# Kernel optimization log

Hardware: AMD Instinct MI355X
Metric: run time of the kernel (lower is better)

The kernel has to match this reference:

```python
import jax, jax.numpy as jnp
import numpy as np

L = 8        # len_prog
E = 8        # experts per layer (uniform dsl_num)
D = 256      # embed_dim
B = 16384    # batch_size
H1, H2 = 64, 32  # MyMLP hidden dims


def setup_inputs() -> dict:
    key = jax.random.key(0)
    ks = jax.random.split(key, 8)
    s1 = 1.0 / np.sqrt(D)
    s2 = 1.0 / np.sqrt(H1)
    s3 = 1.0 / np.sqrt(H2)
    return {
        "src_embeddings": jax.random.normal(ks[0], (B, D), jnp.float32),
        "W1": jax.random.normal(ks[1], (L, E, H1, D), jnp.float32) * s1,
        "b1": jax.random.normal(ks[2], (L, E, H1), jnp.float32) * s1,
        "W2": jax.random.normal(ks[3], (L, E, H2, H1), jnp.float32) * s2,
        "b2": jax.random.normal(ks[4], (L, E, H2), jnp.float32) * s2,
        "W3": jax.random.normal(ks[5], (L, E, D, H2), jnp.float32) * s3,
        "b3": jax.random.normal(ks[6], (L, E, D), jnp.float32) * s3,
        "masks": jax.random.normal(ks[7], (L, B, E), jnp.float32) * 0.1,
    }


def reference(src_embeddings, W1, b1, W2, b2, W3, b3, masks):
    # Per layer: run E small expert MLPs on the same x, then combine with
    # softmax(mask) over the expert axis (torch path: masks=None -> softmax).
    def layer(x, params):
        w1, bb1, w2, bb2, w3, bb3, m = params
        h = jax.nn.relu(jnp.einsum('bd,ehd->beh', x, w1) + bb1)      # [B,E,H1]
        h = jax.nn.relu(jnp.einsum('beh,ekh->bek', h, w2) + bb2)     # [B,E,H2]
        out = jnp.einsum('bek,edk->bed', h, w3) + bb3                # [B,E,D]
        w = jax.nn.softmax(m, axis=-1)                               # [B,E]
        x_new = jnp.einsum('be,bed->bd', w, out)                     # [B,D]
        return x_new, None

    x, _ = jax.lax.scan(layer, src_embeddings, (W1, b1, W2, b2, W3, b3, masks))
    return x
```

## Files before the change

### kernel.cpp

```cpp
#include <hip/hip_runtime.h>
#include <hip/hip_bf16.h>

#define LNUM 8
#define ENUM 8
#define DDIM 256
#define BSZ  16384
#define H1N  64
#define H2N  32

#define BT   64
#define NTHR 512

#define PX   264
#define PH1  72
#define PH2  40
#define PSW  9

#define WS1_OFF 0
#define WS2_OFF 1048576
#define WS3_OFF 1179648

typedef float f32x4 __attribute__((ext_vector_type(4)));
typedef unsigned short u16x8 __attribute__((ext_vector_type(8)));
typedef unsigned short u16x4 __attribute__((ext_vector_type(4)));
typedef __bf16 bf16x8 __attribute__((ext_vector_type(8)));

#define Z4 ((f32x4){0.f, 0.f, 0.f, 0.f})

static __device__ __forceinline__ unsigned short f2bf(float f) {
    unsigned u = __builtin_bit_cast(unsigned, f);
    u += 0x7fffu + ((u >> 16) & 1u);
    return (unsigned short)(u >> 16);
}

static __device__ __forceinline__ f32x4 mfma16(u16x8 a, u16x8 b, f32x4 c) {
    return __builtin_amdgcn_mfma_f32_16x16x32_bf16(
        __builtin_bit_cast(bf16x8, a), __builtin_bit_cast(bf16x8, b), c, 0, 0, 0);
}

__global__ __launch_bounds__(256) void cvt_w_frag(
    const float* __restrict__ w1, const float* __restrict__ w2,
    const float* __restrict__ w3, unsigned short* __restrict__ ws)
{
    int gid = blockIdx.x * 256 + threadIdx.x;
    const float* src;
    unsigned short* dst;
    if (gid < 131072) {
        int s = gid >> 11, rem = gid & 2047;
        int n = rem >> 5, kc = rem & 31;
        int nt = n >> 4, r = n & 15, kt = kc >> 2, q = kc & 3;
        src = w1 + (size_t)gid * 8;
        dst = ws + WS1_OFF + (size_t)s * 16384 + nt * 4096 + kt * 512 + (q * 16 + r) * 8;
    } else if (gid < 147456) {
        int g = gid - 131072;
        int s = g >> 8, rem = g & 255;
        int n = rem >> 3, kc = rem & 7;
        int n2 = n >> 4, r = n & 15, kt = kc >> 2, q = kc & 3;
        src = w2 + (size_t)g * 8;
        dst = ws + WS2_OFF + (size_t)s * 2048 + n2 * 1024 + kt * 512 + (q * 16 + r) * 8;
    } else {
        int g = gid - 147456;
        int s = g >> 10, rem = g & 1023;
        int n = rem >> 2, q = rem & 3;
        int nt = n >> 4, r = n & 15;
        src = w3 + (size_t)g * 8;
        dst = ws + WS3_OFF + (size_t)s * 8192 + nt * 512 + (q * 16 + r) * 8;
    }
    float4 a = *(const float4*)src;
    float4 b = *(const float4*)(src + 4);
    u16x8 p;
    p[0] = f2bf(a.x); p[1] = f2bf(a.y); p[2] = f2bf(a.z); p[3] = f2bf(a.w);
    p[4] = f2bf(b.x); p[5] = f2bf(b.y); p[6] = f2bf(b.z); p[7] = f2bf(b.w);
    *(u16x8*)dst = p;
}

__global__ __launch_bounds__(NTHR, 2) void moe_fused(
    const float* __restrict__ src, const unsigned short* __restrict__ Wf,
    const float* __restrict__ b1, const float* __restrict__ b2,
    const float* __restrict__ b3, const float* __restrict__ masks,
    float* __restrict__ out)
{
    __shared__ __align__(16) unsigned short Xlds[BT * PX];
    __shared__ __align__(16) unsigned short H1T[2][BT * PH1];
    __shared__ __align__(16) unsigned short H2T[2][BT * PH2];
    __shared__ float SWlds[BT * PSW];

    const int tid  = threadIdx.x;
    const int lane = tid & 63;
    const int w    = tid >> 6;
    const int wm   = w >> 2;
    const int wn   = w & 3;
    const int n15  = lane & 15;
    const int q    = lane >> 4;
    const int b0   = blockIdx.x * BT;

    const unsigned short* w1base = Wf + WS1_OFF + wn * 4096 + lane * 8;
    const unsigned short* w2base = Wf + WS2_OFF + wm * 1024 + lane * 8;
    const unsigned short* w3base = Wf + WS3_OFF + wn * 2048 + lane * 8;

    u16x8 xf[2][8];
    f32x4 ACC[2][4];

    auto stage_softmax = [&](int l) {
        if (tid < 64) {
            const float* mp = masks + ((size_t)l * BSZ + b0 + tid) * ENUM;
            float4 m0 = *(const float4*)mp;
            float4 m1 = *(const float4*)(mp + 4);
            float mv[8] = {m0.x, m0.y, m0.z, m0.w, m1.x, m1.y, m1.z, m1.w};
            float mx = mv[0];
            #pragma unroll
            for (int e = 1; e < 8; ++e) mx = fmaxf(mx, mv[e]);
            float s = 0.f;
            #pragma unroll
            for (int e = 0; e < 8; ++e) { mv[e] = expf(mv[e] - mx); s += mv[e]; }
            float inv = 1.f / s;
            #pragma unroll
            for (int e = 0; e < 8; ++e) SWlds[tid * PSW + e] = mv[e] * inv;
        }
    };

    auto acc_init = [&](int l) {
        const float* b3l = b3 + (size_t)l * ENUM * DDIM;
        #pragma unroll
        for (int mt = 0; mt < 2; ++mt)
            #pragma unroll
            for (int nt = 0; nt < 4; ++nt) ACC[mt][nt] = Z4;
        #pragma unroll 2
        for (int e2 = 0; e2 < ENUM; ++e2) {
            float swv[2][4];
            #pragma unroll
            for (int mt = 0; mt < 2; ++mt)
                #pragma unroll
                for (int rg = 0; rg < 4; ++rg)
                    swv[mt][rg] = SWlds[(wm*32 + mt*16 + q*4 + rg) * PSW + e2];
            #pragma unroll
            for (int nt = 0; nt < 4; ++nt) {
                float bv = b3l[e2 * DDIM + wn*64 + nt*16 + n15];
                #pragma unroll
                for (int mt = 0; mt < 2; ++mt)
                    #pragma unroll
                    for (int rg = 0; rg < 4; ++rg)
                        ACC[mt][nt][rg] += swv[mt][rg] * bv;
            }
        }
    };

    auto xf_read = [&]() {
        #pragma unroll
        for (int mt = 0; mt < 2; ++mt)
            #pragma unroll
            for (int kt = 0; kt < 8; ++kt)
                xf[mt][kt] = *(const u16x8*)
                    &Xlds[(wm*32 + mt*16 + n15) * PX + q*8 + kt*32];
    };
    auto x_write = [&]() {
        #pragma unroll
        for (int mt = 0; mt < 2; ++mt)
            #pragma unroll
            for (int nt = 0; nt < 4; ++nt)
                #pragma unroll
                for (int rg = 0; rg < 4; ++rg)
                    Xlds[(wm*32 + mt*16 + q*4 + rg) * PX + wn*64 + nt*16 + n15] =
                        f2bf(ACC[mt][nt][rg]);
    };

    #pragma unroll
    for (int i = 0; i < 4; ++i) {
        int o = (i * NTHR + tid) * 8;
        int r = o >> 8, c = o & 255;
        const float* p = src + (size_t)(b0 + r) * DDIM + c;
        float4 f0 = *(const float4*)(p);
        float4 f1 = *(const float4*)(p + 4);
        u16x8 pk;
        pk[0] = f2bf(f0.x); pk[1] = f2bf(f0.y); pk[2] = f2bf(f0.z); pk[3] = f2bf(f0.w);
        pk[4] = f2bf(f1.x); pk[5] = f2bf(f1.y); pk[6] = f2bf(f1.z); pk[7] = f2bf(f1.w);
        *(u16x8*)&Xlds[r * PX + c] = pk;
    }
    stage_softmax(0);
    __syncthreads();
    xf_read();
    acc_init(0);

    #pragma unroll 1
    for (int ss = 0; ss < LNUM * ENUM / 2; ++ss) {
        const int s0 = 2 * ss, s1 = s0 + 1;
        const int l  = s0 >> 3, e0 = s0 & 7, e1 = s1 & 7;

        u16x8 wfA[8], wfB[8], w2A[2], w2B[2];
        {
            const unsigned short* pA = w1base + (size_t)s0 * 16384;
            const unsigned short* pB = w1base + (size_t)s1 * 16384;
            #pragma unroll
            for (int kt = 0; kt < 8; ++kt) {
                wfA[kt] = *(const u16x8*)(pA + kt * 512);
                wfB[kt] = *(const u16x8*)(pB + kt * 512);
            }
            const unsigned short* q2A = w2base + (size_t)s0 * 2048;
            const unsigned short* q2B = w2base + (size_t)s1 * 2048;
            w2A[0] = *(const u16x8*)(q2A);  w2A[1] = *(const u16x8*)(q2A + 512);
            w2B[0] = *(const u16x8*)(q2B);  w2B[1] = *(const u16x8*)(q2B + 512);
        }
        const float4 bb1A = *(const float4*)(b1 + s0 * 64 + wn * 16 + q * 4);
        const float4 bb1B = *(const float4*)(b1 + s1 * 64 + wn * 16 + q * 4);
        const float4 bb2A = *(const float4*)(b2 + s0 * 32 + wm * 16 + q * 4);
        const float4 bb2B = *(const float4*)(b2 + s1 * 32 + wm * 16 + q * 4);

        f32x4 a1A[2] = {Z4, Z4}, a1B[2] = {Z4, Z4};
        #pragma unroll
        for (int kt = 0; kt < 8; ++kt) {
            a1A[0] = mfma16(wfA[kt], xf[0][kt], a1A[0]);
            a1A[1] = mfma16(wfA[kt], xf[1][kt], a1A[1]);
            a1B[0] = mfma16(wfB[kt], xf[0][kt], a1B[0]);
            a1B[1] = mfma16(wfB[kt], xf[1][kt], a1B[1]);
        }

        u16x8 w3A[4], w3B[4];
        {
            const unsigned short* p3A = w3base + (size_t)s0 * 8192;
            const unsigned short* p3B = w3base + (size_t)s1 * 8192;
            #pragma unroll
            for (int nt = 0; nt < 4; ++nt) {
                w3A[nt] = *(const u16x8*)(p3A + nt * 512);
                w3B[nt] = *(const u16x8*)(p3B + nt * 512);
            }
        }

        #pragma unroll
        for (int mt = 0; mt < 2; ++mt) {
            u16x4 pkA, pkB;
            #pragma unroll
            for (int rg = 0; rg < 4; ++rg) {
                pkA[rg] = f2bf(fmaxf(a1A[mt][rg] + bb1A[rg], 0.f));
                pkB[rg] = f2bf(fmaxf(a1B[mt][rg] + bb1B[rg], 0.f));
            }
            int row = wm*32 + mt*16 + n15;
            *(u16x4*)&H1T[0][row * PH1 + wn*16 + q*4] = pkA;
            *(u16x4*)&H1T[1][row * PH1 + wn*16 + q*4] = pkB;
        }
        __syncthreads();

        f32x4 a2A = Z4, a2B = Z4;
        {
            u16x8 hA0 = *(const u16x8*)&H1T[0][(wn*16 + n15) * PH1 + q*8];
            u16x8 hA1 = *(const u16x8*)&H1T[0][(wn*16 + n15) * PH1 + q*8 + 32];
            u16x8 hB0 = *(const u16x8*)&H1T[1][(wn*16 + n15) * PH1 + q*8];
            u16x8 hB1 = *(const u16x8*)&H1T[1][(wn*16 + n15) * PH1 + q*8 + 32];
            a2A = mfma16(w2A[0], hA0, a2A);
            a2B = mfma16(w2B[0], hB0, a2B);
            a2A = mfma16(w2A[1], hA1, a2A);
            a2B = mfma16(w2B[1], hB1, a2B);
        }
        {
            int row = wn*16 + n15;
            float swA = SWlds[row * PSW + e0];
            float swB = SWlds[row * PSW + e1];
            u16x4 pkA, pkB;
            #pragma unroll
            for (int rg = 0; rg < 4; ++rg) {
                pkA[rg] = f2bf(fmaxf(a2A[rg] + bb2A[rg], 0.f) * swA);
                pkB[rg] = f2bf(fmaxf(a2B[rg] + bb2B[rg], 0.f) * swB);
            }
            *(u16x4*)&H2T[0][row * PH2 + wm*16 + q*4] = pkA;
            *(u16x4*)&H2T[1][row * PH2 + wm*16 + q*4] = pkB;
        }
        __syncthreads();

        {
            u16x8 hA0 = *(const u16x8*)&H2T[0][(wm*32 + n15) * PH2 + q*8];
            u16x8 hA1 = *(const u16x8*)&H2T[0][(wm*32 + 16 + n15) * PH2 + q*8];
            u16x8 hB0 = *(const u16x8*)&H2T[1][(wm*32 + n15) * PH2 + q*8];
            u16x8 hB1 = *(const u16x8*)&H2T[1][(wm*32 + 16 + n15) * PH2 + q*8];
            #pragma unroll
            for (int nt = 0; nt < 4; ++nt) {
                ACC[0][nt] = mfma16(hA0, w3A[nt], ACC[0][nt]);
                ACC[1][nt] = mfma16(hA1, w3A[nt], ACC[1][nt]);
            }
            #pragma unroll
            for (int nt = 0; nt < 4; ++nt) {
                ACC[0][nt] = mfma16(hB0, w3B[nt], ACC[0][nt]);
                ACC[1][nt] = mfma16(hB1, w3B[nt], ACC[1][nt]);
            }
        }

        if (e1 == 7 && l < LNUM - 1) {
            x_write();
            __syncthreads();
            xf_read();
            stage_softmax(l + 1);
            __syncthreads();
            acc_init(l + 1);
        }
    }

    #pragma unroll
    for (int mt = 0; mt < 2; ++mt)
        #pragma unroll
        for (int nt = 0; nt < 4; ++nt)
            #pragma unroll
            for (int rg = 0; rg < 4; ++rg)
                out[(size_t)(b0 + wm*32 + mt*16 + q*4 + rg) * DDIM
                    + wn*64 + nt*16 + n15] = ACC[mt][nt][rg];
}

extern "C" void kernel_launch(void* const* d_in, const int* in_sizes, int n_in,
                              void* d_out, int out_size, void* d_ws, size_t ws_size,
                              hipStream_t stream) {
    const float* src   = (const float*)d_in[0];
    const float* W1    = (const float*)d_in[1];
    const float* b1    = (const float*)d_in[2];
    const float* W2    = (const float*)d_in[3];
    const float* b2    = (const float*)d_in[4];
    const float* W3    = (const float*)d_in[5];
    const float* b3    = (const float*)d_in[6];
    const float* masks = (const float*)d_in[7];
    float* out = (float*)d_out;
    unsigned short* ws = (unsigned short*)d_ws;

    hipLaunchKernelGGL(cvt_w_frag, dim3(832), dim3(256), 0, stream, W1, W2, W3, ws);
    hipLaunchKernelGGL(moe_fused, dim3(BSZ / BT), dim3(NTHR), 0, stream,
                       src, ws, b1, b2, b3, masks, out);
}
```

Baseline: 190.6 us.

## Halve batch tile to 32 rows and remap stage-2 waves per expert

Batch tile shrinks from 64 to 32 rows per block, so each wave now covers one 16-row m-tile instead of two. Stage 2 is rebuilt so each wave-row group handles a single expert of the pair rather than both. Launch bounds rise to 4 blocks per CU, aiming for more resident waves, lower register pressure and twice as many blocks to fill the GPU. In exchange, each block streams the full expert weights for half as many rows, which doubles global/L2 weight traffic per output row and halves MFMA reuse of every weight fragment.

```diff
diff --git a/kernel.cpp b/kernel.cpp
--- a/kernel.cpp
+++ b/kernel.cpp
@@ -8,7 +8,7 @@
 #define H1N  64
 #define H2N  32
 
-#define BT   64
+#define BT   32
 #define NTHR 512
 
 #define PX   264
@@ -74,7 +74,7 @@
     *(u16x8*)dst = p;
 }
 
-__global__ __launch_bounds__(NTHR, 2) void moe_fused(
+__global__ __launch_bounds__(NTHR, 4) void moe_fused(
     const float* __restrict__ src, const unsigned short* __restrict__ Wf,
     const float* __restrict__ b1, const float* __restrict__ b2,
     const float* __restrict__ b3, const float* __restrict__ masks,
@@ -90,19 +90,21 @@
     const int w    = tid >> 6;
     const int wm   = w >> 2;
     const int wn   = w & 3;
+    const int r2   = wn & 1;
+    const int f2   = wn >> 1;
     const int n15  = lane & 15;
     const int q    = lane >> 4;
     const int b0   = blockIdx.x * BT;
 
     const unsigned short* w1base = Wf + WS1_OFF + wn * 4096 + lane * 8;
-    const unsigned short* w2base = Wf + WS2_OFF + wm * 1024 + lane * 8;
+    const unsigned short* w2base = Wf + WS2_OFF + f2 * 1024 + lane * 8;
     const unsigned short* w3base = Wf + WS3_OFF + wn * 2048 + lane * 8;
 
-    u16x8 xf[2][8];
-    f32x4 ACC[2][4];
+    u16x8 xf[8];
+    f32x4 ACC[4];
 
     auto stage_softmax = [&](int l) {
-        if (tid < 64) {
+        if (tid < BT) {
             const float* mp = masks + ((size_t)l * BSZ + b0 + tid) * ENUM;
             float4 m0 = *(const float4*)mp;
             float4 m1 = *(const float4*)(mp + 4);
@@ -122,50 +124,39 @@
     auto acc_init = [&](int l) {
         const float* b3l = b3 + (size_t)l * ENUM * DDIM;
         #pragma unroll
-        for (int mt = 0; mt < 2; ++mt)
-            #pragma unroll
-            for (int nt = 0; nt < 4; ++nt) ACC[mt][nt] = Z4;
+        for (int nt = 0; nt < 4; ++nt) ACC[nt] = Z4;
         #pragma unroll 2
         for (int e2 = 0; e2 < ENUM; ++e2) {
-            float swv[2][4];
-            #pragma unroll
-            for (int mt = 0; mt < 2; ++mt)
-                #pragma unroll
-                for (int rg = 0; rg < 4; ++rg)
-                    swv[mt][rg] = SWlds[(wm*32 + mt*16 + q*4 + rg) * PSW + e2];
+            float swv[4];
+            #pragma unroll
+            for (int rg = 0; rg < 4; ++rg)
+                swv[rg] = SWlds[(wm*16 + q*4 + rg) * PSW + e2];
             #pragma unroll
             for (int nt = 0; nt < 4; ++nt) {
                 float bv = b3l[e2 * DDIM + wn*64 + nt*16 + n15];
                 #pragma unroll
-                for (int mt = 0; mt < 2; ++mt)
-                    #pragma unroll
-                    for (int rg = 0; rg < 4; ++rg)
-                        ACC[mt][nt][rg] += swv[mt][rg] * bv;
+                for (int rg = 0; rg < 4; ++rg)
+                    ACC[nt][rg] += swv[rg] * bv;
             }
         }
     };
 
     auto xf_read = [&]() {
         #pragma unroll
-        for (int mt = 0; mt < 2; ++mt)
-            #pragma unroll
-            for (int kt = 0; kt < 8; ++kt)
-                xf[mt][kt] = *(const u16x8*)
-                    &Xlds[(wm*32 + mt*16 + n15) * PX + q*8 + kt*32];
+        for (int kt = 0; kt < 8; ++kt)
+            xf[kt] = *(const u16x8*)&Xlds[(wm*16 + n15) * PX + q*8 + kt*32];
     };
     auto x_write = [&]() {
         #pragma unroll
-        for (int mt = 0; mt < 2; ++mt)
-            #pragma unroll
-            for (int nt = 0; nt < 4; ++nt)
-                #pragma unroll
-                for (int rg = 0; rg < 4; ++rg)
-                    Xlds[(wm*32 + mt*16 + q*4 + rg) * PX + wn*64 + nt*16 + n15] =
-                        f2bf(ACC[mt][nt][rg]);
+        for (int nt = 0; nt < 4; ++nt)
+            #pragma unroll
+            for (int rg = 0; rg < 4; ++rg)
+                Xlds[(wm*16 + q*4 + rg) * PX + wn*64 + nt*16 + n15] =
+                    f2bf(ACC[nt][rg]);
     };
 
     #pragma unroll
-    for (int i = 0; i < 4; ++i) {
+    for (int i = 0; i < 2; ++i) {
         int o = (i * NTHR + tid) * 8;
         int r = o >> 8, c = o & 255;
         const float* p = src + (size_t)(b0 + r) * DDIM + c;
@@ -184,9 +175,9 @@
     #pragma unroll 1
     for (int ss = 0; ss < LNUM * ENUM / 2; ++ss) {
         const int s0 = 2 * ss, s1 = s0 + 1;
-        const int l  = s0 >> 3, e0 = s0 & 7, e1 = s1 & 7;
-
-        u16x8 wfA[8], wfB[8], w2A[2], w2B[2];
+        const int l  = s0 >> 3, e0 = s0 & 7;
+
+        u16x8 wfA[8], wfB[8], w2f[2];
         {
             const unsigned short* pA = w1base + (size_t)s0 * 16384;
             const unsigned short* pB = w1base + (size_t)s1 * 16384;
@@ -195,23 +186,18 @@
                 wfA[kt] = *(const u16x8*)(pA + kt * 512);
                 wfB[kt] = *(const u16x8*)(pB + kt * 512);
             }
-            const unsigned short* q2A = w2base + (size_t)s0 * 2048;
-            const unsigned short* q2B = w2base + (size_t)s1 * 2048;
-            w2A[0] = *(const u16x8*)(q2A);  w2A[1] = *(const u16x8*)(q2A + 512);
-            w2B[0] = *(const u16x8*)(q2B);  w2B[1] = *(const u16x8*)(q2B + 512);
+            const unsigned short* q2 = w2base + (size_t)(s0 + wm) * 2048;
+            w2f[0] = *(const u16x8*)(q2);  w2f[1] = *(const u16x8*)(q2 + 512);
         }
         const float4 bb1A = *(const float4*)(b1 + s0 * 64 + wn * 16 + q * 4);
         const float4 bb1B = *(const float4*)(b1 + s1 * 64 + wn * 16 + q * 4);
-        const float4 bb2A = *(const float4*)(b2 + s0 * 32 + wm * 16 + q * 4);
-        const float4 bb2B = *(const float4*)(b2 + s1 * 32 + wm * 16 + q * 4);
-
-        f32x4 a1A[2] = {Z4, Z4}, a1B[2] = {Z4, Z4};
+        const float4 bb2  = *(const float4*)(b2 + (s0 + wm) * 32 + f2 * 16 + q * 4);
+
+        f32x4 a1A = Z4, a1B = Z4;
         #pragma unroll
         for (int kt = 0; kt < 8; ++kt) {
-            a1A[0] = mfma16(wfA[kt], xf[0][kt], a1A[0]);
-            a1A[1] = mfma16(wfA[kt], xf[1][kt], a1A[1]);
-            a1B[0] = mfma16(wfB[kt], xf[0][kt], a1B[0]);
-            a1B[1] = mfma16(wfB[kt], xf[1][kt], a1B[1]);
+            a1A = mfma16(wfA[kt], xf[kt], a1A);
+            a1B = mfma16(wfB[kt], xf[kt], a1B);
         }
 
         u16x8 w3A[4], w3B[4];
@@ -225,64 +211,47 @@
             }
         }
 
-        #pragma unroll
-        for (int mt = 0; mt < 2; ++mt) {
+        {
             u16x4 pkA, pkB;
             #pragma unroll
             for (int rg = 0; rg < 4; ++rg) {
-                pkA[rg] = f2bf(fmaxf(a1A[mt][rg] + bb1A[rg], 0.f));
-                pkB[rg] = f2bf(fmaxf(a1B[mt][rg] + bb1B[rg], 0.f));
-            }
-            int row = wm*32 + mt*16 + n15;
+                pkA[rg] = f2bf(fmaxf(a1A[rg] + bb1A[rg], 0.f));
+                pkB[rg] = f2bf(fmaxf(a1B[rg] + bb1B[rg], 0.f));
+            }
+            int row = wm*16 + n15;
             *(u16x4*)&H1T[0][row * PH1 + wn*16 + q*4] = pkA;
             *(u16x4*)&H1T[1][row * PH1 + wn*16 + q*4] = pkB;
         }
         __syncthreads();
 
-        f32x4 a2A = Z4, a2B = Z4;
-        {
-            u16x8 hA0 = *(const u16x8*)&H1T[0][(wn*16 + n15) * PH1 + q*8];
-            u16x8 hA1 = *(const u16x8*)&H1T[0][(wn*16 + n15) * PH1 + q*8 + 32];
-            u16x8 hB0 = *(const u16x8*)&H1T[1][(wn*16 + n15) * PH1 + q*8];
-            u16x8 hB1 = *(const u16x8*)&H1T[1][(wn*16 + n15) * PH1 + q*8 + 32];
-            a2A = mfma16(w2A[0], hA0, a2A);
-            a2B = mfma16(w2B[0], hB0, a2B);
-            a2A = mfma16(w2A[1], hA1, a2A);
-            a2B = mfma16(w2B[1], hB1, a2B);
-        }
-        {
-            int row = wn*16 + n15;
-            float swA = SWlds[row * PSW + e0];
-            float swB = SWlds[row * PSW + e1];
-            u16x4 pkA, pkB;
-            #pragma unroll
-            for (int rg = 0; rg < 4; ++rg) {
-                pkA[rg] = f2bf(fmaxf(a2A[rg] + bb2A[rg], 0.f) * swA);
-                pkB[rg] = f2bf(fmaxf(a2B[rg] + bb2B[rg], 0.f) * swB);
-            }
-            *(u16x4*)&H2T[0][row * PH2 + wm*16 + q*4] = pkA;
-            *(u16x4*)&H2T[1][row * PH2 + wm*16 + q*4] = pkB;
+        {
+            f32x4 a2 = Z4;
+            int hrow = r2*16 + n15;
+            u16x8 h0 = *(const u16x8*)&H1T[wm][hrow * PH1 + q*8];
+            u16x8 h1 = *(const u16x8*)&H1T[wm][hrow * PH1 + q*8 + 32];
+            a2 = mfma16(w2f[0], h0, a2);
+            a2 = mfma16(w2f[1], h1, a2);
+            float sw = SWlds[hrow * PSW + e0 + wm];
+            u16x4 pk;
+            #pragma unroll
+            for (int rg = 0; rg < 4; ++rg)
+                pk[rg] = f2bf(fmaxf(a2[rg] + bb2[rg], 0.f) * sw);
+            *(u16x4*)&H2T[wm][hrow * PH2 + f2*16 + q*4] = pk;
         }
         __syncthreads();
 
         {
-            u16x8 hA0 = *(const u16x8*)&H2T[0][(wm*32 + n15) * PH2 + q*8];
-            u16x8 hA1 = *(const u16x8*)&H2T[0][(wm*32 + 16 + n15) * PH2 + q*8];
-            u16x8 hB0 = *(const u16x8*)&H2T[1][(wm*32 + n15) * PH2 + q*8];
-            u16x8 hB1 = *(const u16x8*)&H2T[1][(wm*32 + 16 + n15) * PH2 + q*8];
-            #pragma unroll
-            for (int nt = 0; nt < 4; ++nt) {
-                ACC[0][nt] = mfma16(hA0, w3A[nt], ACC[0][nt]);
-                ACC[1][nt] = mfma16(hA1, w3A[nt], ACC[1][nt]);
-            }
-            #pragma unroll
-            for (int nt = 0; nt < 4; ++nt) {
-                ACC[0][nt] = mfma16(hB0, w3B[nt], ACC[0][nt]);
-                ACC[1][nt] = mfma16(hB1, w3B[nt], ACC[1][nt]);
-            }
-        }
-
-        if (e1 == 7 && l < LNUM - 1) {
+            u16x8 hA = *(const u16x8*)&H2T[0][(wm*16 + n15) * PH2 + q*8];
+            u16x8 hB = *(const u16x8*)&H2T[1][(wm*16 + n15) * PH2 + q*8];
+            #pragma unroll
+            for (int nt = 0; nt < 4; ++nt)
+                ACC[nt] = mfma16(hA, w3A[nt], ACC[nt]);
+            #pragma unroll
+            for (int nt = 0; nt < 4; ++nt)
+                ACC[nt] = mfma16(hB, w3B[nt], ACC[nt]);
+        }
+
+        if ((ss & 3) == 3 && l < LNUM - 1) {
             x_write();
             __syncthreads();
             xf_read();
@@ -293,13 +262,11 @@
     }
 
     #pragma unroll
-    for (int mt = 0; mt < 2; ++mt)
-        #pragma unroll
-        for (int nt = 0; nt < 4; ++nt)
-            #pragma unroll
-            for (int rg = 0; rg < 4; ++rg)
-                out[(size_t)(b0 + wm*32 + mt*16 + q*4 + rg) * DDIM
-                    + wn*64 + nt*16 + n15] = ACC[mt][nt][rg];
+    for (int nt = 0; nt < 4; ++nt)
+        #pragma unroll
+        for (int rg = 0; rg < 4; ++rg)
+            out[(size_t)(b0 + wm*16 + q*4 + rg) * DDIM
+                + wn*64 + nt*16 + n15] = ACC[nt][rg];
 }
 
 extern "C" void kernel_launch(void* const* d_in, const int* in_sizes, int n_in,
```

New measurement: 244.7 us. 1.28x slower.

## Prefetch next expert-pair W1/W2 fragments into registers and use LDS-only barriers

Applied to the files above, without the earlier changes.

W1 and W2 weight fragments for the next expert pair are now loaded into registers during the current iteration, after their last use, so global-load latency overlaps with the compute and barriers of the current pair. __syncthreads is replaced by a custom barrier that waits only on lgkmcnt (LDS traffic), not on outstanding global loads, so the prefetches stay in flight across barriers. On the final iteration the prefetch reads past the weight buffer into the W3 region, which is harmless but wasteful. Register pressure rises, which may cause spills at 512 threads.

```diff
diff --git a/kernel.cpp b/kernel.cpp
--- a/kernel.cpp
+++ b/kernel.cpp
@@ -36,6 +36,12 @@
 static __device__ __forceinline__ f32x4 mfma16(u16x8 a, u16x8 b, f32x4 c) {
     return __builtin_amdgcn_mfma_f32_16x16x32_bf16(
         __builtin_bit_cast(bf16x8, a), __builtin_bit_cast(bf16x8, b), c, 0, 0, 0);
+}
+
+static __device__ __forceinline__ void lbar() {
+    asm volatile("s_waitcnt lgkmcnt(0)" ::: "memory");
+    __builtin_amdgcn_s_barrier();
+    asm volatile("" ::: "memory");
 }
 
 __global__ __launch_bounds__(256) void cvt_w_frag(
@@ -100,6 +106,8 @@
 
     u16x8 xf[2][8];
     f32x4 ACC[2][4];
+    u16x8 wfA[8], wfB[8];
+    u16x8 w2A[2], w2B[2];
 
     auto stage_softmax = [&](int l) {
         if (tid < 64) {
@@ -177,7 +185,21 @@
         *(u16x8*)&Xlds[r * PX + c] = pk;
     }
     stage_softmax(0);
-    __syncthreads();
+
+    {
+        const unsigned short* pA = w1base;
+        const unsigned short* pB = w1base + 16384;
+        #pragma unroll
+        for (int kt = 0; kt < 8; ++kt) {
+            wfA[kt] = *(const u16x8*)(pA + kt * 512);
+            wfB[kt] = *(const u16x8*)(pB + kt * 512);
+        }
+        const unsigned short* q2A = w2base;
+        const unsigned short* q2B = w2base + 2048;
+        w2A[0] = *(const u16x8*)(q2A);  w2A[1] = *(const u16x8*)(q2A + 512);
+        w2B[0] = *(const u16x8*)(q2B);  w2B[1] = *(const u16x8*)(q2B + 512);
+    }
+    lbar();
     xf_read();
     acc_init(0);
 
@@ -186,20 +208,6 @@
         const int s0 = 2 * ss, s1 = s0 + 1;
         const int l  = s0 >> 3, e0 = s0 & 7, e1 = s1 & 7;
 
-        u16x8 wfA[8], wfB[8], w2A[2], w2B[2];
-        {
-            const unsigned short* pA = w1base + (size_t)s0 * 16384;
-            const unsigned short* pB = w1base + (size_t)s1 * 16384;
-            #pragma unroll
-            for (int kt = 0; kt < 8; ++kt) {
-                wfA[kt] = *(const u16x8*)(pA + kt * 512);
-                wfB[kt] = *(const u16x8*)(pB + kt * 512);
-            }
-            const unsigned short* q2A = w2base + (size_t)s0 * 2048;
-            const unsigned short* q2B = w2base + (size_t)s1 * 2048;
-            w2A[0] = *(const u16x8*)(q2A);  w2A[1] = *(const u16x8*)(q2A + 512);
-            w2B[0] = *(const u16x8*)(q2B);  w2B[1] = *(const u16x8*)(q2B + 512);
-        }
         const float4 bb1A = *(const float4*)(b1 + s0 * 64 + wn * 16 + q * 4);
         const float4 bb1B = *(const float4*)(b1 + s1 * 64 + wn * 16 + q * 4);
         const float4 bb2A = *(const float4*)(b2 + s0 * 32 + wm * 16 + q * 4);
@@ -225,6 +233,16 @@
             }
         }
 
+        {
+            const unsigned short* pA = w1base + (size_t)(s0 + 2) * 16384;
+            const unsigned short* pB = w1base + (size_t)(s1 + 2) * 16384;
+            #pragma unroll
+            for (int kt = 0; kt < 8; ++kt) {
+                wfA[kt] = *(const u16x8*)(pA + kt * 512);
+                wfB[kt] = *(const u16x8*)(pB + kt * 512);
+            }
+        }
+
         #pragma unroll
         for (int mt = 0; mt < 2; ++mt) {
             u16x4 pkA, pkB;
@@ -237,7 +255,7 @@
             *(u16x4*)&H1T[0][row * PH1 + wn*16 + q*4] = pkA;
             *(u16x4*)&H1T[1][row * PH1 + wn*16 + q*4] = pkB;
         }
-        __syncthreads();
+        lbar();
 
         f32x4 a2A = Z4, a2B = Z4;
         {
@@ -250,6 +268,14 @@
             a2A = mfma16(w2A[1], hA1, a2A);
             a2B = mfma16(w2B[1], hB1, a2B);
         }
+
+        {
+            const unsigned short* q2A = w2base + (size_t)(s0 + 2) * 2048;
+            const unsigned short* q2B = w2base + (size_t)(s1 + 2) * 2048;
+            w2A[0] = *(const u16x8*)(q2A);  w2A[1] = *(const u16x8*)(q2A + 512);
+            w2B[0] = *(const u16x8*)(q2B);  w2B[1] = *(const u16x8*)(q2B + 512);
+        }
+
         {
             int row = wn*16 + n15;
             float swA = SWlds[row * PSW + e0];
@@ -263,7 +289,7 @@
             *(u16x4*)&H2T[0][row * PH2 + wm*16 + q*4] = pkA;
             *(u16x4*)&H2T[1][row * PH2 + wm*16 + q*4] = pkB;
         }
-        __syncthreads();
+        lbar();
 
         {
             u16x8 hA0 = *(const u16x8*)&H2T[0][(wm*32 + n15) * PH2 + q*8];
@@ -284,10 +310,10 @@
 
         if (e1 == 7 && l < LNUM - 1) {
             x_write();
-            __syncthreads();
+            lbar();
             xf_read();
             stage_softmax(l + 1);
-            __syncthreads();
+            lbar();
             acc_init(l + 1);
         }
     }
```

Measured after the change: 200.4 us. 5.1% more time.
